# Performance work log

Measured on AMD Instinct MI355X. Metric: run time of the kernel, lower is better.

The kernel has to match this reference:

```python
import jax, jax.numpy as jnp
import numpy as np

N, D, V = 4096, 2048, 65536
IGNORE_INDEX = -100


def setup_inputs() -> dict:
    key = jax.random.key(0)
    k1, k2, k3 = jax.random.split(key, 3)
    e = jax.random.normal(k1, (N, D), dtype=jnp.float32)
    c = jax.random.normal(k2, (V, D), dtype=jnp.float32) * (D ** -0.5)
    targets = jax.random.randint(k3, (N,), 0, V, dtype=jnp.int64)
    # sprinkle some ignore_index entries to exercise masking
    targets = jnp.where(jnp.arange(N) % 97 == 0, IGNORE_INDEX, targets)
    return {"e": e, "c": c, "targets": targets}


def reference(e, c, targets):
    # logits = e @ c^T  -> [N, V] (the big intermediate CCE avoids materializing)
    logits = jnp.einsum("nd,vd->nv", e, c)
    lse = jax.nn.logsumexp(logits, axis=-1)  # [N]
    valid = targets != IGNORE_INDEX
    safe_t = jnp.where(valid, targets, 0)
    tgt_logit = jnp.take_along_axis(logits, safe_t[:, None], axis=-1)[:, 0]
    nll = jnp.where(valid, lse - tgt_logit, 0.0)
    count = jnp.maximum(jnp.sum(valid), 1)
    return jnp.sum(nll) / count.astype(nll.dtype)
```

## Files before the change

kernel.cpp:

```cpp
#include <hip/hip_runtime.h>
#include <hip/hip_bf16.h>
#include <hip/hip_fp8.h>

typedef __bf16 bf16_t;
typedef bf16_t bf16x8 __attribute__((ext_vector_type(8)));
typedef float f32x4 __attribute__((ext_vector_type(4)));
typedef float f32x16 __attribute__((ext_vector_type(16)));
typedef int   i32x4  __attribute__((ext_vector_type(4)));
typedef int   i32x8  __attribute__((ext_vector_type(8)));

#define N_ROWS 4096
#define DIM    2048
#define VOCAB  65536
#define IGN    (-100)

#define BM 256
#define BN 256
#define BK 128
#define NT (DIM / BK)
#define NUNITS (4 * NT)
#define SCALE1 0x7F7F7F7F

#define GLOAD_LDS16(gp, lp)                                                  \
  __builtin_amdgcn_global_load_lds(                                          \
      (const __attribute__((address_space(1))) void*)(gp),                   \
      (__attribute__((address_space(3))) void*)(lp), 16, 0, 0)

__global__ __launch_bounds__(256)
void cvt_fp8(const float* __restrict__ src, unsigned char* __restrict__ dst,
             long n16, float scale) {
  long i = (long)blockIdx.x * 256 + threadIdx.x;
  long stride = (long)gridDim.x * 256;
  for (; i < n16; i += stride) {
    const float4* s = reinterpret_cast<const float4*>(src) + i * 4;
    union { unsigned char b[16]; i32x4 v; } o;
#pragma unroll
    for (int q = 0; q < 4; ++q) {
      float4 a = s[q];
      o.b[q * 4 + 0] = __hip_fp8_e4m3(a.x * scale).__x;
      o.b[q * 4 + 1] = __hip_fp8_e4m3(a.y * scale).__x;
      o.b[q * 4 + 2] = __hip_fp8_e4m3(a.z * scale).__x;
      o.b[q * 4 + 3] = __hip_fp8_e4m3(a.w * scale).__x;
    }
    *reinterpret_cast<i32x4*>(dst + i * 16) = o.v;
  }
}

__global__ __launch_bounds__(512, 2)
void lce_gemm_fp8(const unsigned char* __restrict__ E8,
                  const unsigned char* __restrict__ C8,
                  float* __restrict__ sumexp) {
  extern __shared__ unsigned char lds[];
  const int tid = threadIdx.x;
  const int lane = tid & 63, wid = tid >> 6;
  const int wr = wid >> 2, wc = wid & 3;
  const int l31 = lane & 31, lh = lane >> 5;

  const int bid = blockIdx.x;
  const int wg = (bid & 7) * (((N_ROWS / BM) * (VOCAB / BN)) / 8) + (bid >> 3);
  const int brow = (wg & (N_ROWS / BM - 1)) * BM;
  const int bcol = (wg / (N_ROWS / BM)) * BN;

  const int g0 = wid * 64 + lane;
  const int g1 = 512 + g0;
  const int prel0 = g0 * 16;
  const int prel1 = g1 * 16;
  auto mkgoff = [&](int g) {
    int slab = g >> 7, chunk = (g >> 5) & 3, r = g & 31;
    return (size_t)(slab * 32 + r) * DIM + (size_t)(chunk * 16);
  };
  const size_t goff0 = mkgoff(g0), goff1 = mkgoff(g1);

  const unsigned char* Ebase = E8 + (size_t)brow * DIM;
  const unsigned char* Cbase = C8 + (size_t)bcol * DIM;

  auto stage = [&](int ug) {
    const unsigned char* gb = ((ug & 1) ? Cbase : Ebase) +
                              (ug >> 2) * BK + ((ug >> 1) & 1) * 64;
    unsigned char* lb = lds + (ug & 7) * 16384;
    GLOAD_LDS16(gb + goff0, lb + prel0);
    GLOAD_LDS16(gb + goff1, lb + prel1);
  };

  auto read_frag = [&](const unsigned char* U, int s) -> i32x8 {
    const unsigned char* p = U + s * 2048 + lh * 1024 + l31 * 16;
    i32x4 lo = *reinterpret_cast<const i32x4*>(p);
    i32x4 hi = *reinterpret_cast<const i32x4*>(p + 512);
    return __builtin_shufflevector(lo, hi, 0, 1, 2, 3, 4, 5, 6, 7);
  };

  f32x16 acc[4][2];
#pragma unroll
  for (int mi = 0; mi < 4; ++mi)
#pragma unroll
    for (int ni = 0; ni < 2; ++ni)
#pragma unroll
      for (int r = 0; r < 16; ++r) acc[mi][ni][r] = 0.f;

  stage(0); stage(1); stage(2); stage(3); stage(4); stage(5); stage(7);
  asm volatile("s_waitcnt vmcnt(6)" ::: "memory");
  __builtin_amdgcn_s_barrier();

  i32x8 af[2], bfr[2];

  for (int T = 0; T < NT; ++T) {
    const unsigned char* base = lds + (T & 1) * 65536;
#pragma unroll
    for (int ph = 0; ph < 4; ++ph) {
      const int ks = ph >> 1, mq = ph & 1;
      const unsigned char* aU = base + ks * 32768;
      const unsigned char* bU = aU + 16384;
      if (mq == 0) {
#pragma unroll
        for (int ni = 0; ni < 2; ++ni)
          bfr[ni] = read_frag(bU, wc * 2 + ni);
#pragma unroll
        for (int mi = 0; mi < 2; ++mi)
          af[mi] = read_frag(aU, wr * 4 + mi);
      } else {
#pragma unroll
        for (int mi = 0; mi < 2; ++mi)
          af[mi] = read_frag(aU, wr * 4 + 2 + mi);
      }
      __builtin_amdgcn_sched_barrier(0);
      const int sug = 4 * T + ((ph == 0) ? 6 : (ph == 1) ? 9 : (ph == 2) ? 8 : 11);
      if (sug < NUNITS) stage(sug);
      asm volatile("s_waitcnt lgkmcnt(0)" ::: "memory");
      __builtin_amdgcn_sched_barrier(0);
      __builtin_amdgcn_s_setprio(1);
#pragma unroll
      for (int mi = 0; mi < 2; ++mi)
#pragma unroll
        for (int ni = 0; ni < 2; ++ni)
          acc[mq * 2 + mi][ni] = __builtin_amdgcn_mfma_scale_f32_32x32x64_f8f6f4(
              af[mi], bfr[ni], acc[mq * 2 + mi][ni],
              0, 0,
              0, SCALE1,
              0, SCALE1);
      __builtin_amdgcn_s_setprio(0);
      if (ph == 3 && T < NT - 1) {
        if (T < NT - 2) asm volatile("s_waitcnt vmcnt(6)" ::: "memory");
        else            asm volatile("s_waitcnt vmcnt(0)" ::: "memory");
      }
      __builtin_amdgcn_s_barrier();
    }
  }

#pragma unroll
  for (int mi = 0; mi < 4; ++mi) {
    float p[16];
#pragma unroll
    for (int r = 0; r < 16; ++r)
      p[r] = __expf(acc[mi][0][r] * 0.125f) + __expf(acc[mi][1][r] * 0.125f);
#pragma unroll
    for (int m = 1; m < 32; m <<= 1)
#pragma unroll
      for (int r = 0; r < 16; ++r) p[r] += __shfl_xor(p[r], m, 64);
    if (l31 == 0) {
#pragma unroll
      for (int r = 0; r < 16; ++r) {
        const int row = brow + wr * 128 + mi * 32 + (r & 3) + 8 * (r >> 2) + 4 * lh;
        atomicAdd(&sumexp[row], p[r]);
      }
    }
  }
}

#define FBM 128
#define FBN 128
#define FBK 64
#define FNK (DIM / FBK)
#define FTHREADS 512

__global__ __launch_bounds__(FTHREADS, 4)
void lce_gemm_f32(const float* __restrict__ E, const float* __restrict__ C,
                  float* __restrict__ sumexp) {
  extern __shared__ unsigned char lds[];
  const int tid  = threadIdx.x;
  const int brow = blockIdx.x * FBM;
  const int bcol = blockIdx.y * FBN;

  float4 ra[4], rb[4];
  auto ld = [&](int k0) {
#pragma unroll
    for (int i = 0; i < 4; ++i) {
      int f = tid + i * FTHREADS;
      int r = f >> 4;
      int c = (f & 15) << 2;
      ra[i] = *reinterpret_cast<const float4*>(&E[(size_t)(brow + r) * DIM + k0 + c]);
      rb[i] = *reinterpret_cast<const float4*>(&C[(size_t)(bcol + r) * DIM + k0 + c]);
    }
  };
  auto st = [&](int buf) {
    unsigned char* a = lds + buf * 32768;
    unsigned char* b = a + 16384;
#pragma unroll
    for (int i = 0; i < 4; ++i) {
      int f  = tid + i * FTHREADS;
      int r  = f >> 4;
      int cbb = (f & 15) << 3;
      int off = r * 128 + (cbb ^ ((r & 7) << 4));
      union { bf16_t h[4]; unsigned long long u; } pa, pb;
      pa.h[0] = (bf16_t)ra[i].x; pa.h[1] = (bf16_t)ra[i].y;
      pa.h[2] = (bf16_t)ra[i].z; pa.h[3] = (bf16_t)ra[i].w;
      pb.h[0] = (bf16_t)rb[i].x; pb.h[1] = (bf16_t)rb[i].y;
      pb.h[2] = (bf16_t)rb[i].z; pb.h[3] = (bf16_t)rb[i].w;
      *reinterpret_cast<unsigned long long*>(a + off) = pa.u;
      *reinterpret_cast<unsigned long long*>(b + off) = pb.u;
    }
  };

  f32x4 acc[4][2];
#pragma unroll
  for (int mi = 0; mi < 4; ++mi)
#pragma unroll
    for (int ni = 0; ni < 2; ++ni) acc[mi][ni] = (f32x4){0.f, 0.f, 0.f, 0.f};

  const int lane = tid & 63, wid = tid >> 6;
  const int wr = wid >> 2, wc = wid & 3;
  const int l15 = lane & 15, lg = lane >> 4;
  const int swz = (l15 & 7) << 4;

  auto comp = [&](int buf) {
    const unsigned char* a = lds + buf * 32768;
    const unsigned char* b = a + 16384;
#pragma unroll
    for (int kk = 0; kk < 2; ++kk) {
      const int cbase = (kk * 64 + lg * 16) ^ swz;
      bf16x8 af[4], bfr[2];
#pragma unroll
      for (int mi = 0; mi < 4; ++mi)
        af[mi] = *reinterpret_cast<const bf16x8*>(
            a + (wr * 64 + mi * 16 + l15) * 128 + cbase);
#pragma unroll
      for (int ni = 0; ni < 2; ++ni)
        bfr[ni] = *reinterpret_cast<const bf16x8*>(
            b + (wc * 32 + ni * 16 + l15) * 128 + cbase);
#pragma unroll
      for (int mi = 0; mi < 4; ++mi)
#pragma unroll
        for (int ni = 0; ni < 2; ++ni)
          acc[mi][ni] = __builtin_amdgcn_mfma_f32_16x16x32_bf16(
              af[mi], bfr[ni], acc[mi][ni], 0, 0, 0);
    }
  };

  ld(0);
  st(0);
  for (int kt = 0; kt < FNK; ++kt) {
    __syncthreads();
    if (kt + 1 < FNK) ld((kt + 1) * FBK);
    comp(kt & 1);
    if (kt + 1 < FNK) st((kt + 1) & 1);
  }

#pragma unroll
  for (int mi = 0; mi < 4; ++mi) {
    float p[4];
#pragma unroll
    for (int j = 0; j < 4; ++j)
      p[j] = __expf(acc[mi][0][j]) + __expf(acc[mi][1][j]);
#pragma unroll
    for (int m = 1; m < 16; m <<= 1)
#pragma unroll
      for (int j = 0; j < 4; ++j) p[j] += __shfl_xor(p[j], m, 64);
    if (l15 == 0) {
      int row = brow + wr * 64 + mi * 16 + lg * 4;
#pragma unroll
      for (int j = 0; j < 4; ++j) atomicAdd(&sumexp[row + j], p[j]);
    }
  }
}

__global__ __launch_bounds__(256)
void lce_tgt(const float* __restrict__ E, const float* __restrict__ C,
             const int* __restrict__ T, float* __restrict__ tgt) {
  int w = (int)((blockIdx.x * blockDim.x + threadIdx.x) >> 6);
  int lane = threadIdx.x & 63;
  if (w >= N_ROWS) return;
  int t = T[w];
  float s = 0.f;
  if (t != IGN) {
    const float4* er = reinterpret_cast<const float4*>(E + (size_t)w * DIM);
    const float4* cr = reinterpret_cast<const float4*>(C + (size_t)t * DIM);
#pragma unroll
    for (int i = 0; i < DIM / 4 / 64; ++i) {
      float4 a = er[lane + i * 64];
      float4 b = cr[lane + i * 64];
      s = fmaf(a.x, b.x, s); s = fmaf(a.y, b.y, s);
      s = fmaf(a.z, b.z, s); s = fmaf(a.w, b.w, s);
    }
#pragma unroll
    for (int m = 1; m < 64; m <<= 1) s += __shfl_xor(s, m, 64);
  }
  if (lane == 0) tgt[w] = s;
}

__global__ __launch_bounds__(256)
void lce_finalize(const float* __restrict__ sumexp, const float* __restrict__ tgt,
                  const int* __restrict__ T, float* __restrict__ out) {
  int tid = threadIdx.x;
  float nll = 0.f, cnt = 0.f;
  for (int n = tid; n < N_ROWS; n += 256) {
    if (T[n] != IGN) {
      nll += logf(sumexp[n]) - tgt[n];
      cnt += 1.f;
    }
  }
#pragma unroll
  for (int m = 1; m < 64; m <<= 1) {
    nll += __shfl_xor(nll, m, 64);
    cnt += __shfl_xor(cnt, m, 64);
  }
  __shared__ float sn[4], sc[4];
  if ((tid & 63) == 0) { sn[tid >> 6] = nll; sc[tid >> 6] = cnt; }
  __syncthreads();
  if (tid == 0) {
    float a = 0.f, b = 0.f;
#pragma unroll
    for (int i = 0; i < 4; ++i) { a += sn[i]; b += sc[i]; }
    out[0] = a / fmaxf(b, 1.f);
  }
}

extern "C" void kernel_launch(void* const* d_in, const int* in_sizes, int n_in,
                              void* d_out, int out_size, void* d_ws, size_t ws_size,
                              hipStream_t stream) {
  const float* E = (const float*)d_in[0];
  const float* C = (const float*)d_in[1];
  const int*   T = (const int*)d_in[2];
  float* out = (float*)d_out;

  unsigned char* ws = (unsigned char*)d_ws;
  float* sumexp = (float*)ws;
  float* tgt    = (float*)(ws + 16384);
  unsigned char* E8 = ws + 32768;
  unsigned char* C8 = E8 + (size_t)N_ROWS * DIM;

  const size_t need = 32768 + (size_t)N_ROWS * DIM + (size_t)VOCAB * DIM;

  hipMemsetAsync(sumexp, 0, N_ROWS * sizeof(float), stream);

  if (ws_size >= need) {
    cvt_fp8<<<2048, 256, 0, stream>>>(E, E8, (long)N_ROWS * DIM / 16, 1.0f);
    cvt_fp8<<<2048, 256, 0, stream>>>(C, C8, (long)VOCAB * DIM / 16, 8.0f);
    lce_gemm_fp8<<<dim3((N_ROWS / BM) * (VOCAB / BN)), 512, 131072, stream>>>(E8, C8, sumexp);
  } else {
    lce_gemm_f32<<<dim3(N_ROWS / FBM, VOCAB / FBN), FTHREADS, 65536, stream>>>(E, C, sumexp);
  }

  lce_tgt<<<dim3((N_ROWS * 64) / 256), 256, 0, stream>>>(E, C, T, tgt);
  lce_finalize<<<dim3(1), 256, 0, stream>>>(sumexp, tgt, T, out);
}
```

Measured before the change: 952.5 us.

## Swizzle LDS fragment layout and merge MFMA phases into two per K-tile

Changes the global-to-LDS staging address mapping to an XOR-swizzled layout and matches it in the fragment reads, aiming to reduce LDS bank conflicts. It also collapses the four per-tile phases into two, loading all four A fragments at once and issuing two stage units per phase. This removes two barriers per K-tile at the cost of more fragment registers and a shallower prefetch window, with staging order and vmcnt waits adjusted to match.

New measurement: 865.5 us, median of 2. 9.1% less time.

```diff
diff --git a/kernel.cpp b/kernel.cpp
--- a/kernel.cpp
+++ b/kernel.cpp
@@ -66,8 +66,9 @@
   const int prel0 = g0 * 16;
   const int prel1 = g1 * 16;
   auto mkgoff = [&](int g) {
-    int slab = g >> 7, chunk = (g >> 5) & 3, r = g & 31;
-    return (size_t)(slab * 32 + r) * DIM + (size_t)(chunk * 16);
+    int w = g >> 6, i = g & 63;
+    return (size_t)(w * 16 + (i >> 2)) * DIM +
+           (size_t)((((i & 3) ^ ((i >> 3) & 3)) << 4));
   };
   const size_t goff0 = mkgoff(g0), goff1 = mkgoff(g1);
 
@@ -82,10 +83,12 @@
     GLOAD_LDS16(gb + goff1, lb + prel1);
   };
 
+  const int sw = (l31 >> 1) & 3;
   auto read_frag = [&](const unsigned char* U, int s) -> i32x8 {
-    const unsigned char* p = U + s * 2048 + lh * 1024 + l31 * 16;
-    i32x4 lo = *reinterpret_cast<const i32x4*>(p);
-    i32x4 hi = *reinterpret_cast<const i32x4*>(p + 512);
+    const unsigned char* p =
+        U + s * 2048 + (l31 >> 4) * 1024 + (l31 & 15) * 64;
+    i32x4 lo = *reinterpret_cast<const i32x4*>(p + (((lh * 2)     ^ sw) << 4));
+    i32x4 hi = *reinterpret_cast<const i32x4*>(p + (((lh * 2 + 1) ^ sw) << 4));
     return __builtin_shufflevector(lo, hi, 0, 1, 2, 3, 4, 5, 6, 7);
   };
 
@@ -97,49 +100,43 @@
 #pragma unroll
       for (int r = 0; r < 16; ++r) acc[mi][ni][r] = 0.f;
 
-  stage(0); stage(1); stage(2); stage(3); stage(4); stage(5); stage(7);
-  asm volatile("s_waitcnt vmcnt(6)" ::: "memory");
+  stage(0); stage(1); stage(2); stage(3); stage(4); stage(5);
+  asm volatile("s_waitcnt vmcnt(4)" ::: "memory");
   __builtin_amdgcn_s_barrier();
 
-  i32x8 af[2], bfr[2];
+  i32x8 af[4], bfr[2];
 
   for (int T = 0; T < NT; ++T) {
     const unsigned char* base = lds + (T & 1) * 65536;
 #pragma unroll
-    for (int ph = 0; ph < 4; ++ph) {
-      const int ks = ph >> 1, mq = ph & 1;
+    for (int ks = 0; ks < 2; ++ks) {
       const unsigned char* aU = base + ks * 32768;
       const unsigned char* bU = aU + 16384;
-      if (mq == 0) {
-#pragma unroll
-        for (int ni = 0; ni < 2; ++ni)
-          bfr[ni] = read_frag(bU, wc * 2 + ni);
-#pragma unroll
-        for (int mi = 0; mi < 2; ++mi)
-          af[mi] = read_frag(aU, wr * 4 + mi);
-      } else {
-#pragma unroll
-        for (int mi = 0; mi < 2; ++mi)
-          af[mi] = read_frag(aU, wr * 4 + 2 + mi);
-      }
+#pragma unroll
+      for (int ni = 0; ni < 2; ++ni)
+        bfr[ni] = read_frag(bU, wc * 2 + ni);
+#pragma unroll
+      for (int mi = 0; mi < 4; ++mi)
+        af[mi] = read_frag(aU, wr * 4 + mi);
       __builtin_amdgcn_sched_barrier(0);
-      const int sug = 4 * T + ((ph == 0) ? 6 : (ph == 1) ? 9 : (ph == 2) ? 8 : 11);
-      if (sug < NUNITS) stage(sug);
+      const int ug = 4 * T + 6 + ks * 2;
+      if (ug < NUNITS) stage(ug);
+      if (ug + 1 < NUNITS) stage(ug + 1);
       asm volatile("s_waitcnt lgkmcnt(0)" ::: "memory");
       __builtin_amdgcn_sched_barrier(0);
       __builtin_amdgcn_s_setprio(1);
 #pragma unroll
-      for (int mi = 0; mi < 2; ++mi)
+      for (int mi = 0; mi < 4; ++mi)
 #pragma unroll
         for (int ni = 0; ni < 2; ++ni)
-          acc[mq * 2 + mi][ni] = __builtin_amdgcn_mfma_scale_f32_32x32x64_f8f6f4(
-              af[mi], bfr[ni], acc[mq * 2 + mi][ni],
+          acc[mi][ni] = __builtin_amdgcn_mfma_scale_f32_32x32x64_f8f6f4(
+              af[mi], bfr[ni], acc[mi][ni],
               0, 0,
               0, SCALE1,
               0, SCALE1);
       __builtin_amdgcn_s_setprio(0);
-      if (ph == 3 && T < NT - 1) {
-        if (T < NT - 2) asm volatile("s_waitcnt vmcnt(6)" ::: "memory");
+      if (ks == 1 && T < NT - 1) {
+        if (T < NT - 2) asm volatile("s_waitcnt vmcnt(4)" ::: "memory");
         else            asm volatile("s_waitcnt vmcnt(0)" ::: "memory");
       }
       __builtin_amdgcn_s_barrier();
```
